# Optimization experiments

Measured on AMD Instinct MI355X. Metric: run time of the kernel, lower is better.

Reference implementation:

```python
import jax, jax.numpy as jnp
import numpy as np

IM_MAX = 1.0
IM_SIZE = 128
N_THRESHOLDS = 64


def _thresholds():
    # end = im_size * sqrt(2) // 2  (float32 math, floor-div) -> 90.0
    end = np.float32(np.float32(IM_SIZE) * np.sqrt(np.float32(2.0))) // np.float32(2.0)
    t = np.linspace(2.0, float(end), N_THRESHOLDS, dtype=np.float32)
    return np.round(t).astype(np.int32)  # half-to-even, matches torch.round


def _masks():
    # stack of circular low-pass masks, one per threshold: [T, H, W]
    crow, ccol = IM_SIZE // 2, IM_SIZE // 2
    y = np.arange(IM_SIZE)[:, None]
    x = np.arange(IM_SIZE)[None, :]
    r2 = (x - ccol) ** 2 + (y - crow) ** 2  # [H, W]
    thr = _thresholds().astype(np.int64)
    m = (r2[None, :, :] <= (thr[:, None, None] ** 2)).astype(np.float32)
    return jnp.asarray(m)


def setup_inputs() -> dict:
    key = jax.random.key(0)
    k1, k2 = jax.random.split(key)
    shape = (256, 3, IM_SIZE, IM_SIZE)
    prediction = jax.random.uniform(k1, shape, dtype=jnp.float32)
    gt = jax.random.uniform(k2, shape, dtype=jnp.float32)
    return {"prediction": prediction, "gt": gt}


def reference(prediction, gt):
    # Single FFT pass on each input (original redundantly recomputes per threshold,
    # but mask is 0/1 so masked-diff energy = mask * |pred_f - gt_f|^2).
    pf = jnp.fft.fftshift(jnp.fft.fft2(prediction), axes=(-2, -1))  # [B,C,H,W] c64
    gf = jnp.fft.fftshift(jnp.fft.fft2(gt), axes=(-2, -1))
    diff = pf - gf
    sq_err = diff.real ** 2 + diff.imag ** 2  # |.|^2, [B,C,H,W] f32
    masks = _masks()  # [T,H,W]
    # sum_sq_error per (batch, threshold): sum over C,H,W with mask
    sum_sq = jnp.einsum('thw,bchw->bt', masks, sq_err)  # [B,T]
    n_pixels = IM_SIZE * IM_SIZE
    const = 20.0 * jnp.log10(jnp.float32(IM_MAX * n_pixels))
    cf_psnr = const - 10.0 * jnp.log10(sum_sq)
    return cf_psnr
```

## Files before the change

kernel.cpp:

```cpp
#include <hip/hip_runtime.h>
#include <hip/hip_fp16.h>

#define IMG 128
#define NPIX (IMG * IMG)
#define NT 64
#define LSU 129
#define ZCH (64 * LSU)

__device__ __constant__ int c_thr[NT] = {
    2, 3, 5, 6, 8, 9, 10, 12, 13, 15, 16, 17, 19, 20, 22, 23,
    24, 26, 27, 29, 30, 31, 33, 34, 36, 37, 38, 40, 41, 43, 44, 45,
    47, 48, 49, 51, 52, 54, 55, 56, 58, 59, 61, 62, 63, 65, 66, 68,
    69, 70, 72, 73, 75, 76, 77, 79, 80, 82, 83, 84, 86, 87, 89, 90};

__device__ __forceinline__ int rev7(int x) { return (int)(__brev((unsigned)x) >> 25); }

__device__ __forceinline__ unsigned packh2(float x, float y) {
    __half2 h = __floats2half2_rn(x, y);
    return *reinterpret_cast<unsigned*>(&h);
}
__device__ __forceinline__ float2 unpackh2(unsigned u) {
    __half2 h;
    *reinterpret_cast<unsigned*>(&h) = u;
    return __half22float2(h);
}

__device__ __forceinline__ float x1f(float v) {
    return __int_as_float(__builtin_amdgcn_mov_dpp(__float_as_int(v), 0xB1, 0xF, 0xF, true));
}
__device__ __forceinline__ float x2f(float v) {
    return __int_as_float(__builtin_amdgcn_mov_dpp(__float_as_int(v), 0x4E, 0xF, 0xF, true));
}
__device__ __forceinline__ float x4f(float v) {
    return __int_as_float(__builtin_amdgcn_ds_swizzle(__float_as_int(v), 0x101F));
}
__device__ __forceinline__ float x8f(float v) {
    return __int_as_float(__builtin_amdgcn_mov_dpp(__float_as_int(v), 0x128, 0xF, 0xF, true));
}

__global__ __launch_bounds__(1024) void fused_psnr_kernel(const float* __restrict__ pred,
                                                          const float* __restrict__ gt,
                                                          float* __restrict__ out) {
    __shared__ unsigned s_z[3 * ZCH];
    __shared__ float s_hist[NT];
    __shared__ int s_rc2bin[91];

    const int tid = threadIdx.x;
    const int lane = tid & 63;
    const int wave = tid >> 6;
    const int l = lane & 15;
    const int g = lane >> 4;
    const int b = blockIdx.x;

    if (tid < 64) s_hist[tid] = 0.0f;
    if (tid >= 64 && tid < 64 + 91) {
        const int rc = tid - 64;
        int t = 0;
        while (t < 63 && c_thr[t] < rc) ++t;
        s_rc2bin[rc] = t;
    }

    const float K = -6.2831853071795864769f * (1.0f / 128.0f);
    float c64[4], s64[4], c32[2], s32[2], c16v, s16v;
#pragma unroll
    for (int j = 0; j < 4; ++j) sincosf(K * (float)(16 * j + l), &s64[j], &c64[j]);
    sincosf(K * (float)(2 * l), &s32[0], &c32[0]);
    sincosf(K * (float)(2 * l + 32), &s32[1], &c32[1]);
    sincosf(K * (float)(4 * l), &s16v, &c16v);
    float c8v, s8v, c4v, s4v, c2v, s2v;
    sincosf(K * (float)((l & 8) ? (l & 7) * 8 : 0), &s8v, &c8v);
    sincosf(K * (float)((l & 4) ? (l & 3) * 16 : 0), &s4v, &c4v);
    sincosf(K * (float)((l & 2) ? (l & 1) * 32 : 0), &s2v, &c2v);
    const float sg8 = (l & 8) ? -1.0f : 1.0f;
    const float sg4 = (l & 4) ? -1.0f : 1.0f;
    const float sg2 = (l & 2) ? -1.0f : 1.0f;
    const float sg1 = (l & 1) ? -1.0f : 1.0f;

    float dy2f[8];
    const int r4 = ((l & 1) << 3) | ((l & 2) << 1) | ((l & 4) >> 1) | ((l & 8) >> 3);
#pragma unroll
    for (int j = 0; j < 8; ++j) {
        const int fy = (((j & 1) << 2) | (j & 2) | ((j & 4) >> 2)) | (r4 << 3);
        const int dy = (fy < 64) ? fy : 128 - fy;
        dy2f[j] = (float)(dy * dy);
    }

    auto bfly = [](float& ar, float& ai, float& br, float& bi, float wc, float wsn) {
        const float dr = ar - br, di = ai - bi;
        ar += br; ai += bi;
        br = dr * wc - di * wsn;
        bi = dr * wsn + di * wc;
    };

    auto fft = [&](float* vr, float* vi) {
#pragma unroll
        for (int j = 0; j < 4; ++j) bfly(vr[j], vi[j], vr[j + 4], vi[j + 4], c64[j], s64[j]);
        bfly(vr[0], vi[0], vr[2], vi[2], c32[0], s32[0]);
        bfly(vr[1], vi[1], vr[3], vi[3], c32[1], s32[1]);
        bfly(vr[4], vi[4], vr[6], vi[6], c32[0], s32[0]);
        bfly(vr[5], vi[5], vr[7], vi[7], c32[1], s32[1]);
#pragma unroll
        for (int j = 0; j < 8; j += 2) bfly(vr[j], vi[j], vr[j + 1], vi[j + 1], c16v, s16v);
#pragma unroll
        for (int j = 0; j < 8; ++j) {
            const float pr = x8f(vr[j]), pi = x8f(vi[j]);
            const float xr = fmaf(sg8, vr[j], pr), xi = fmaf(sg8, vi[j], pi);
            vr[j] = xr * c8v - xi * s8v;
            vi[j] = xr * s8v + xi * c8v;
        }
#pragma unroll
        for (int j = 0; j < 8; ++j) {
            const float pr = x4f(vr[j]), pi = x4f(vi[j]);
            const float xr = fmaf(sg4, vr[j], pr), xi = fmaf(sg4, vi[j], pi);
            vr[j] = xr * c4v - xi * s4v;
            vi[j] = xr * s4v + xi * c4v;
        }
#pragma unroll
        for (int j = 0; j < 8; ++j) {
            const float pr = x2f(vr[j]), pi = x2f(vi[j]);
            const float xr = fmaf(sg2, vr[j], pr), xi = fmaf(sg2, vi[j], pi);
            vr[j] = xr * c2v - xi * s2v;
            vi[j] = xr * s2v + xi * c2v;
        }
#pragma unroll
        for (int j = 0; j < 8; ++j) {
            const float pr = x1f(vr[j]), pi = x1f(vi[j]);
            vr[j] = fmaf(sg1, vr[j], pr);
            vi[j] = fmaf(sg1, vi[j], pi);
        }
    };

    const size_t ibase = (size_t)b * 3 * NPIX;

    for (int t3 = 0; t3 < 3; ++t3) {
        const int T = t3 * 16 + wave;
        const int ch = T >> 4;
        const int Bp = T & 15;
        const int q = (Bp & 7) | ((Bp >> 3) << 5);
        const int r = q + 8 * g;
        const float* pe = pred + ibase + (size_t)ch * NPIX + (size_t)(2 * r) * IMG;
        const float* ge = gt + ibase + (size_t)ch * NPIX + (size_t)(2 * r) * IMG;
        float vr[8], vi[8];
#pragma unroll
        for (int j = 0; j < 8; ++j) {
            const int o = 16 * j + l;
            vr[j] = 0.5f * (pe[o] - ge[o]);
            vi[j] = 0.5f * (pe[IMG + o] - ge[IMG + o]);
        }
        fft(vr, vi);
        const int zb = ch * ZCH + r * LSU;
#pragma unroll
        for (int j = 0; j < 8; ++j) s_z[zb + 16 * j + l] = packh2(vr[j], vi[j]);
    }
    __syncthreads();

    for (int t3 = 0; t3 < 4; ++t3) {
        const int T = t3 * 16 + wave;
        if (T >= 51) break;
        const int ch = T / 17;
        const int t = T - ch * 17;
        int u;
        float wf;
        if (t < 16) {
            u = (t & 3) + ((t >> 2) << 4) + 4 * g;
            wf = (u == 0) ? 1.0f : 2.0f;
        } else {
            u = 64;
            wf = (g == 0) ? 1.0f : 0.0f;
        }
        const int c1 = rev7(u);
        const int c2 = rev7((128 - u) & 127);
        const int zb = ch * ZCH;
        const int zr = l >> 1;
        const int odd = l & 1;
        float vr[8], vi[8];
#pragma unroll
        for (int j = 0; j < 8; ++j) {
            const int rowo = zb + (8 * j + zr) * LSU;
            const float2 A = unpackh2(s_z[rowo + c1]);
            const float2 B = unpackh2(s_z[rowo + c2]);
            vr[j] = odd ? (A.y + B.y) : (A.x + B.x);
            vi[j] = odd ? (B.x - A.x) : (A.y - B.y);
        }
        fft(vr, vi);
        const float u2f = (float)(u * u);
#pragma unroll
        for (int j = 0; j < 8; ++j) {
            const float r2f = dy2f[j] + u2f;
            if (wf != 0.0f && r2f <= 8100.0f) {
                const int rc = (int)ceilf(sqrtf(r2f) - 3e-4f);
                atomicAdd(&s_hist[s_rc2bin[rc]], wf * (vr[j] * vr[j] + vi[j] * vi[j]));
            }
        }
    }
    __syncthreads();

    if (tid < 64) {
        float cum = 0.0f;
        for (int j = 0; j <= tid; ++j) cum += s_hist[j];
        out[b * NT + tid] = 84.2883987849f - 10.0f * log10f(cum);
    }
}

extern "C" void kernel_launch(void* const* d_in, const int* in_sizes, int n_in,
                              void* d_out, int out_size, void* d_ws, size_t ws_size,
                              hipStream_t stream) {
    const float* pred = (const float*)d_in[0];
    const float* gt = (const float*)d_in[1];
    float* out = (float*)d_out;
    fused_psnr_kernel<<<256, 1024, 0, stream>>>(pred, gt, out);
}
```

Measured before the change: 58.06 us.

## Double-buffer row and column loads, per-wave histograms, DPP lane-xor-4

Row-FFT global loads and column-FFT shared-memory loads are now issued one tile ahead into register buffers, so load latency can overlap with the FFT math of the previous tile. The single shared histogram becomes 16 per-wave histograms, summed at the end, to cut contention on shared-memory atomics. The ds_swizzle used for the lane-xor-4 exchange is replaced by two DPP moves. The extra register buffers increase pressure under the 1024-thread launch bound and may cause spills or lower occupancy.

```diff
diff --git a/kernel.cpp b/kernel.cpp
--- a/kernel.cpp
+++ b/kernel.cpp
@@ -31,8 +31,14 @@
 __device__ __forceinline__ float x2f(float v) {
     return __int_as_float(__builtin_amdgcn_mov_dpp(__float_as_int(v), 0x4E, 0xF, 0xF, true));
 }
+__device__ __forceinline__ float x3f(float v) {
+    return __int_as_float(__builtin_amdgcn_mov_dpp(__float_as_int(v), 0x1B, 0xF, 0xF, true));
+}
+__device__ __forceinline__ float x7f(float v) {
+    return __int_as_float(__builtin_amdgcn_mov_dpp(__float_as_int(v), 0x141, 0xF, 0xF, true));
+}
 __device__ __forceinline__ float x4f(float v) {
-    return __int_as_float(__builtin_amdgcn_ds_swizzle(__float_as_int(v), 0x101F));
+    return x7f(x3f(v));
 }
 __device__ __forceinline__ float x8f(float v) {
     return __int_as_float(__builtin_amdgcn_mov_dpp(__float_as_int(v), 0x128, 0xF, 0xF, true));
@@ -42,7 +48,7 @@
                                                           const float* __restrict__ gt,
                                                           float* __restrict__ out) {
     __shared__ unsigned s_z[3 * ZCH];
-    __shared__ float s_hist[NT];
+    __shared__ float s_h[16][66];
     __shared__ int s_rc2bin[91];
 
     const int tid = threadIdx.x;
@@ -52,12 +58,11 @@
     const int g = lane >> 4;
     const int b = blockIdx.x;
 
-    if (tid < 64) s_hist[tid] = 0.0f;
-    if (tid >= 64 && tid < 64 + 91) {
-        const int rc = tid - 64;
+    for (int i = tid; i < 16 * 66; i += 1024) (&s_h[0][0])[i] = 0.0f;
+    if (tid < 91) {
         int t = 0;
-        while (t < 63 && c_thr[t] < rc) ++t;
-        s_rc2bin[rc] = t;
+        while (t < 63 && c_thr[t] < tid) ++t;
+        s_rc2bin[tid] = t;
     }
 
     const float K = -6.2831853071795864769f * (1.0f / 128.0f);
@@ -76,15 +81,6 @@
     const float sg2 = (l & 2) ? -1.0f : 1.0f;
     const float sg1 = (l & 1) ? -1.0f : 1.0f;
 
-    float dy2f[8];
-    const int r4 = ((l & 1) << 3) | ((l & 2) << 1) | ((l & 4) >> 1) | ((l & 8) >> 3);
-#pragma unroll
-    for (int j = 0; j < 8; ++j) {
-        const int fy = (((j & 1) << 2) | (j & 2) | ((j & 4) >> 2)) | (r4 << 3);
-        const int dy = (fy < 64) ? fy : 128 - fy;
-        dy2f[j] = (float)(dy * dy);
-    }
-
     auto bfly = [](float& ar, float& ai, float& br, float& bi, float wc, float wsn) {
         const float dr = ar - br, di = ai - bi;
         ar += br; ai += bi;
@@ -132,31 +128,76 @@
 
     const size_t ibase = (size_t)b * 3 * NPIX;
 
-    for (int t3 = 0; t3 < 3; ++t3) {
-        const int T = t3 * 16 + wave;
+    auto ldRow = [&](int T, float* buf) {
         const int ch = T >> 4;
         const int Bp = T & 15;
         const int q = (Bp & 7) | ((Bp >> 3) << 5);
         const int r = q + 8 * g;
         const float* pe = pred + ibase + (size_t)ch * NPIX + (size_t)(2 * r) * IMG;
         const float* ge = gt + ibase + (size_t)ch * NPIX + (size_t)(2 * r) * IMG;
+#pragma unroll
+        for (int j = 0; j < 8; ++j) {
+            const int o = 16 * j + l;
+            buf[j] = pe[o];
+            buf[8 + j] = pe[IMG + o];
+            buf[16 + j] = ge[o];
+            buf[24 + j] = ge[IMG + o];
+        }
+    };
+    auto doRow = [&](int T, const float* buf) {
+        const int ch = T >> 4;
+        const int Bp = T & 15;
+        const int q = (Bp & 7) | ((Bp >> 3) << 5);
+        const int r = q + 8 * g;
         float vr[8], vi[8];
 #pragma unroll
         for (int j = 0; j < 8; ++j) {
-            const int o = 16 * j + l;
-            vr[j] = 0.5f * (pe[o] - ge[o]);
-            vi[j] = 0.5f * (pe[IMG + o] - ge[IMG + o]);
+            vr[j] = 0.5f * (buf[j] - buf[16 + j]);
+            vi[j] = 0.5f * (buf[8 + j] - buf[24 + j]);
         }
         fft(vr, vi);
         const int zb = ch * ZCH + r * LSU;
 #pragma unroll
         for (int j = 0; j < 8; ++j) s_z[zb + 16 * j + l] = packh2(vr[j], vi[j]);
+    };
+
+    {
+        float bufA[32], bufB[32];
+        ldRow(wave, bufA);
+        ldRow(16 + wave, bufB);
+        doRow(wave, bufA);
+        ldRow(32 + wave, bufA);
+        doRow(16 + wave, bufB);
+        doRow(32 + wave, bufA);
     }
     __syncthreads();
 
-    for (int t3 = 0; t3 < 4; ++t3) {
-        const int T = t3 * 16 + wave;
-        if (T >= 51) break;
+    float dy2f[8];
+    const int r4 = ((l & 1) << 3) | ((l & 2) << 1) | ((l & 4) >> 1) | ((l & 8) >> 3);
+#pragma unroll
+    for (int j = 0; j < 8; ++j) {
+        const int fy = (((j & 1) << 2) | (j & 2) | ((j & 4) >> 2)) | (r4 << 3);
+        const int dy = (fy < 64) ? fy : 128 - fy;
+        dy2f[j] = (float)(dy * dy);
+    }
+    const int zr = l >> 1;
+    const int odd = l & 1;
+
+    auto ldZf = [&](int T, unsigned* raw) {
+        const int ch = T / 17;
+        const int t = T - ch * 17;
+        const int u = (t < 16) ? ((t & 3) + ((t >> 2) << 4) + 4 * g) : 64;
+        const int c1 = rev7(u);
+        const int c2 = rev7((128 - u) & 127);
+        const int zb = ch * ZCH;
+#pragma unroll
+        for (int j = 0; j < 8; ++j) {
+            const int rowo = zb + (8 * j + zr) * LSU;
+            raw[2 * j] = s_z[rowo + c1];
+            raw[2 * j + 1] = s_z[rowo + c2];
+        }
+    };
+    auto doCol = [&](int T, const unsigned* raw) {
         const int ch = T / 17;
         const int t = T - ch * 17;
         int u;
@@ -168,17 +209,11 @@
             u = 64;
             wf = (g == 0) ? 1.0f : 0.0f;
         }
-        const int c1 = rev7(u);
-        const int c2 = rev7((128 - u) & 127);
-        const int zb = ch * ZCH;
-        const int zr = l >> 1;
-        const int odd = l & 1;
         float vr[8], vi[8];
 #pragma unroll
         for (int j = 0; j < 8; ++j) {
-            const int rowo = zb + (8 * j + zr) * LSU;
-            const float2 A = unpackh2(s_z[rowo + c1]);
-            const float2 B = unpackh2(s_z[rowo + c2]);
+            const float2 A = unpackh2(raw[2 * j]);
+            const float2 B = unpackh2(raw[2 * j + 1]);
             vr[j] = odd ? (A.y + B.y) : (A.x + B.x);
             vi[j] = odd ? (B.x - A.x) : (A.y - B.y);
         }
@@ -189,15 +224,31 @@
             const float r2f = dy2f[j] + u2f;
             if (wf != 0.0f && r2f <= 8100.0f) {
                 const int rc = (int)ceilf(sqrtf(r2f) - 3e-4f);
-                atomicAdd(&s_hist[s_rc2bin[rc]], wf * (vr[j] * vr[j] + vi[j] * vi[j]));
+                atomicAdd(&s_h[wave][s_rc2bin[rc]], wf * (vr[j] * vr[j] + vi[j] * vi[j]));
             }
         }
+    };
+
+    {
+        unsigned zA[16], zB[16];
+        ldZf(wave, zA);
+        ldZf(wave + 16, zB);
+        doCol(wave, zA);
+        ldZf(wave + 32, zA);
+        doCol(wave + 16, zB);
+        if (wave + 48 < 51) ldZf(wave + 48, zB);
+        doCol(wave + 32, zA);
+        if (wave + 48 < 51) doCol(wave + 48, zB);
     }
     __syncthreads();
 
     if (tid < 64) {
+        float tot = 0.0f;
+#pragma unroll
+        for (int w = 0; w < 16; ++w) tot += s_h[w][tid];
+        s_h[0][tid] = tot;
         float cum = 0.0f;
-        for (int j = 0; j <= tid; ++j) cum += s_hist[j];
+        for (int j = 0; j <= tid; ++j) cum += s_h[0][j];
         out[b * NT + tid] = 84.2883987849f - 10.0f * log10f(cum);
     }
 }
```

After: 58.03 us. About the same (-0.1%).
